# Kernel optimization log

Measured on AMD Instinct MI355X. Metric: run time of the kernel, lower is better.

Reference implementation:

```python
import jax, jax.numpy as jnp
import numpy as np

DIM = -1
ALPHA = 1.5
N_ITERS = 100


def _p(z):
    # p(z) = clamp(z, min=0) ** (1 / (alpha - 1)); for alpha=1.5 this is square
    return jnp.maximum(z, 0.0) ** (1.0 / (ALPHA - 1.0))


def entmax_bisect(X):
    """Bisection search for the entmax threshold tau (entmax_bisect, alpha=1.5)."""
    am1 = ALPHA - 1.0
    d = X.shape[DIM]
    Xs = X * am1                                   # scaled logits
    max_val = jnp.max(Xs, axis=DIM, keepdims=True)
    tau_lo = max_val - 1.0                         # gp(1) = 1**(alpha-1) = 1
    tau_hi = max_val - (1.0 / d) ** am1            # gp(1/d)
    f_lo = jnp.sum(_p(Xs - tau_lo), axis=DIM, keepdims=True) - 1.0
    dm0 = tau_hi - tau_lo

    def body(i, carry):
        tau_lo, dm, _ = carry
        dm = dm * 0.5
        tau_m = tau_lo + dm
        p_m = _p(Xs - tau_m)
        f_m = jnp.sum(p_m, axis=DIM, keepdims=True) - 1.0
        tau_lo = jnp.where(f_m * f_lo >= 0.0, tau_m, tau_lo)
        return (tau_lo, dm, p_m)

    p0 = jnp.zeros_like(Xs)
    _, _, p_m = jax.lax.fori_loop(0, N_ITERS, body, (tau_lo, dm0, p0))
    # ensure_sum_one normalization (as in the entmax library forward)
    return p_m / jnp.sum(p_m, axis=DIM, keepdims=True)


def setup_inputs() -> dict:
    key = jax.random.key(0)
    x = jax.random.normal(key, (2, 1024, 32000), dtype=jnp.float32)
    return {"x": x}


def reference(x):
    # LogEntmaxBisect.forward: log(entmax_bisect(x, dim, alpha, iters))
    # zero-probability entries yield -inf, matching torch.log(0.)
    return jnp.log(entmax_bisect(x))
```

## Files before the change

### kernel.cpp

```cpp
#include <hip/hip_runtime.h>
#include <float.h>
#include <math.h>

#define D_DIM   32000
#define NT      256
#define CHUNKS  (D_DIM / 4)
#define KITER   ((CHUNKS + NT - 1) / NT)
#define NG4     (KITER / 4)
#define NWAVES  (NT / 64)
#define CAPW    1200

typedef float f32x4 __attribute__((ext_vector_type(4)));
typedef unsigned long long ull;

__device__ __forceinline__ float waveReduceSum(float v) {
#pragma unroll
    for (int m = 32; m >= 1; m >>= 1) v += __shfl_xor(v, m, 64);
    return v;
}

__device__ __forceinline__ float waveReduceMax(float v) {
#pragma unroll
    for (int m = 32; m >= 1; m >>= 1) v = fmaxf(v, __shfl_xor(v, m, 64));
    return v;
}

__device__ __forceinline__ float scrub_finite(float v) {
    const unsigned u = __float_as_uint(v);
    if ((u & 0x7f800000u) == 0x7f800000u) return -FLT_MAX;
    return v;
}

__device__ __forceinline__ float4 ldg4(const float4* __restrict__ p, int c) {
    if (c < CHUNKS) return p[c];
    float4 r; r.x = r.y = r.z = r.w = -FLT_MAX;
    return r;
}

__global__ __launch_bounds__(NT, 8)
void entmax_log_fused(const float* __restrict__ x, float* __restrict__ out, int rows)
{
    const int row = blockIdx.x;
    if (row >= rows) return;
    const size_t base = (size_t)row * D_DIM;
    const float4* __restrict__ xr4 = reinterpret_cast<const float4*>(x + base);
    float* __restrict__ orow = out + base;

    __shared__ __align__(16) float s_pool[NWAVES * CAPW];
    __shared__ float s_red[NWAVES];
    __shared__ int   s_cnt[NWAVES];
    __shared__ int   s_flag;
    __shared__ float2 s_ts;

    const int lane = threadIdx.x & 63;
    const int wv   = threadIdx.x >> 6;
    float* __restrict__ wpool = s_pool + wv * CAPW;
    const ull lmask = (1ull << lane) - 1ull;

    if (threadIdx.x == 0) s_flag = 0;
    __syncthreads();

    float runL  = -FLT_MAX;
    float waveM = -FLT_MAX;
    float pendR = -FLT_MAX;
    int n = 0;
    bool ovf = false;

    float4 cur[4], nxt[4];
#pragma unroll
    for (int j = 0; j < 4; ++j) cur[j] = ldg4(xr4, threadIdx.x + j * NT);

    for (int g = 0; g < NG4; ++g) {
        if (g + 1 < NG4) {
#pragma unroll
            for (int j = 0; j < 4; ++j)
                nxt[j] = ldg4(xr4, threadIdx.x + ((g + 1) * 4 + j) * NT);
        }
        float z[16];
#pragma unroll
        for (int j = 0; j < 4; ++j) {
            z[4 * j + 0] = cur[j].x; z[4 * j + 1] = cur[j].y;
            z[4 * j + 2] = cur[j].z; z[4 * j + 3] = cur[j].w;
        }
        float cm = z[0];
#pragma unroll
        for (int i = 1; i < 16; ++i) cm = fmaxf(cm, z[i]);
        runL = fmaxf(runL, cm);
        if ((g & 1) == 0) {
            waveM = fmaxf(waveM, pendR);
            pendR = waveReduceMax(runL);
        }

        float thrL = fmaxf(runL, waveM) - 2.0f;
        ull msk[16];
        int tot = 0;
#pragma unroll
        for (int j = 0; j < 16; ++j) {
            msk[j] = __ballot(z[j] > thrL);
            tot += __popcll(msk[j]);
        }
        if (tot) {
            if (n + tot > CAPW) {
                const float wfresh = waveReduceMax(runL);
                waveM = fmaxf(waveM, wfresh);
                const float thrW = wfresh - 2.0f;
                int nn = 0;
                for (int i = 0; i < n; i += 64) {
                    const float v = (i + lane < n) ? wpool[i + lane] : -FLT_MAX;
                    const ull km = __ballot(v > thrW);
                    const int r = __popcll(km & lmask);
                    if (v > thrW) wpool[nn + r] = v;
                    nn += __popcll(km);
                }
                n = nn;
                thrL = fmaxf(runL, waveM) - 2.0f;
                tot = 0;
#pragma unroll
                for (int j = 0; j < 16; ++j) {
                    msk[j] = __ballot(z[j] > thrL);
                    tot += __popcll(msk[j]);
                }
            }
            if (n + tot > CAPW) {
                ovf = true;
            } else {
#pragma unroll
                for (int j = 0; j < 16; ++j) {
                    if (z[j] > thrL) {
                        const int r = __popcll(msk[j] & lmask);
                        wpool[n + r] = z[j];
                    }
                    n += __popcll(msk[j]);
                }
            }
        }
#pragma unroll
        for (int j = 0; j < 4; ++j) cur[j] = nxt[j];
    }
    if (ovf && lane == 0) s_flag = 1;

    if (lane == 0) s_red[wv] = waveReduceMax(runL);
    __syncthreads();
    const float max_val = fmaxf(fmaxf(s_red[0], s_red[1]), fmaxf(s_red[2], s_red[3]));
    const int flag = s_flag;
    __syncthreads();

    const float u_lo0 = max_val - 2.0f;
    const float u_hi  = max_val - 0.011180339887498949f;

    if (!flag) {
        {
            int nn = 0;
            for (int i = 0; i < n; i += 64) {
                const float v = (i + lane < n) ? wpool[i + lane] : -FLT_MAX;
                const ull km = __ballot(v > u_lo0);
                const int r = __popcll(km & lmask);
                if (v > u_lo0) wpool[nn + r] = v;
                nn += __popcll(km);
            }
            if (lane == 0) s_cnt[wv] = nn;
        }
        __syncthreads();

        if (wv == 0) {
            const int n0 = s_cnt[0], n1 = s_cnt[1], n2 = s_cnt[2], n3 = s_cnt[3];

#define POOL_SCAN(uv, acc)                                                     \
            do {                                                               \
                const float* __restrict__ pp0 = s_pool;                        \
                for (int i = lane; i < n0; i += 64) {                          \
                    const float t = fmaxf(pp0[i] - (uv), 0.0f);                \
                    acc = fmaf(t, t, acc);                                     \
                }                                                              \
                const float* __restrict__ pp1 = s_pool + CAPW;                 \
                for (int i = lane; i < n1; i += 64) {                          \
                    const float t = fmaxf(pp1[i] - (uv), 0.0f);                \
                    acc = fmaf(t, t, acc);                                     \
                }                                                              \
                const float* __restrict__ pp2 = s_pool + 2 * CAPW;             \
                for (int i = lane; i < n2; i += 64) {                          \
                    const float t = fmaxf(pp2[i] - (uv), 0.0f);                \
                    acc = fmaf(t, t, acc);                                     \
                }                                                              \
                const float* __restrict__ pp3 = s_pool + 3 * CAPW;             \
                for (int i = lane; i < n3; i += 64) {                          \
                    const float t = fmaxf(pp3[i] - (uv), 0.0f);                \
                    acc = fmaf(t, t, acc);                                     \
                }                                                              \
            } while (0)

            float u_lo = u_lo0;
            float fl = 0.0f;
            POOL_SCAN(u_lo, fl);
            fl = waveReduceSum(fl) - 4.0f;

            float dm = u_hi - u_lo;
            float u_m = u_lo;
            float s_v = 4.0f;
            for (int it = 0; it < 100; ++it) {
                dm *= 0.5f;
                u_m = u_lo + dm;
                const bool fixed = (u_m == u_lo);
                float a = 0.0f;
                POOL_SCAN(u_m, a);
                a = waveReduceSum(a);
                s_v = a;
                if ((a - 4.0f) * fl >= 0.0f) u_lo = u_m;
                if (fixed) break;
            }
#undef POOL_SCAN
            if (lane == 0) { s_ts.x = u_m; s_ts.y = s_v; }
        }
        __syncthreads();
    } else {
        float u_lo = u_lo0;
        float acc = 0.0f;
        for (int k = 0; k < KITER; ++k) {
            const int c = threadIdx.x + k * NT;
            if (c < CHUNKS) {
                const float4 v = xr4[c];
                float t;
                t = fmaxf(v.x - u_lo, 0.0f); acc = fmaf(t, t, acc);
                t = fmaxf(v.y - u_lo, 0.0f); acc = fmaf(t, t, acc);
                t = fmaxf(v.z - u_lo, 0.0f); acc = fmaf(t, t, acc);
                t = fmaxf(v.w - u_lo, 0.0f); acc = fmaf(t, t, acc);
            }
        }
        acc = waveReduceSum(acc);
        if (lane == 0) s_red[wv] = acc;
        __syncthreads();
        const float f_lo = (s_red[0] + s_red[1] + s_red[2] + s_red[3]) - 4.0f;
        __syncthreads();

        float dm = u_hi - u_lo;
        float u_m = u_lo;
        float s_v = 4.0f;
        for (int it = 0; it < 100; ++it) {
            dm *= 0.5f;
            u_m = u_lo + dm;
            const bool fixed = (u_m == u_lo);
            float a = 0.0f;
            for (int k = 0; k < KITER; ++k) {
                const int c = threadIdx.x + k * NT;
                if (c < CHUNKS) {
                    const float4 v = xr4[c];
                    float t;
                    t = fmaxf(v.x - u_m, 0.0f); a = fmaf(t, t, a);
                    t = fmaxf(v.y - u_m, 0.0f); a = fmaf(t, t, a);
                    t = fmaxf(v.z - u_m, 0.0f); a = fmaf(t, t, a);
                    t = fmaxf(v.w - u_m, 0.0f); a = fmaf(t, t, a);
                }
            }
            a = waveReduceSum(a);
            if (lane == 0) s_red[wv] = a;
            __syncthreads();
            const float s = s_red[0] + s_red[1] + s_red[2] + s_red[3];
            __syncthreads();
            s_v = s;
            if ((s - 4.0f) * f_lo >= 0.0f) u_lo = u_m;
            if (fixed) break;
        }
        if (threadIdx.x == 0) { s_ts.x = u_m; s_ts.y = s_v; }
        __syncthreads();
    }

    const float u_m = s_ts.x;
    const float inv_sv = 1.0f / s_ts.y;
    for (int k = 0; k < KITER; ++k) {
        const int c = threadIdx.x + k * NT;
        if (c < CHUNKS) {
            const float4 v = xr4[c];
            f32x4 o;
            {
                const float t = fmaxf(v.x - u_m, 0.0f);
                o.x = scrub_finite(__logf(fmaxf(t * t, 1e-35f) * inv_sv));
            }
            {
                const float t = fmaxf(v.y - u_m, 0.0f);
                o.y = scrub_finite(__logf(fmaxf(t * t, 1e-35f) * inv_sv));
            }
            {
                const float t = fmaxf(v.z - u_m, 0.0f);
                o.z = scrub_finite(__logf(fmaxf(t * t, 1e-35f) * inv_sv));
            }
            {
                const float t = fmaxf(v.w - u_m, 0.0f);
                o.w = scrub_finite(__logf(fmaxf(t * t, 1e-35f) * inv_sv));
            }
            __builtin_nontemporal_store(o, reinterpret_cast<f32x4*>(orow) + c);
        }
    }
}

extern "C" void kernel_launch(void* const* d_in, const int* in_sizes, int n_in,
                              void* d_out, int out_size, void* d_ws, size_t ws_size,
                              hipStream_t stream) {
    const float* x = (const float*)d_in[0];
    float* out = (float*)d_out;
    const int rows = in_sizes[0] / D_DIM;
    entmax_log_fused<<<dim3(rows), dim3(NT), 0, stream>>>(x, out, rows);
}
```

Measured before the change: 145.3 us.

## Replace pool bisection with Newton iteration on threshold; nontemporal loads in output pass

On the pooled-candidate path, the up-to-100-step bisection is replaced by a Newton iteration that accumulates both sum(t^2) and sum(t) per pass and steps the threshold by g/(2*S1), clamped at u_hi, for at most 24 iterations. This aims to cut the number of serial single-wave scans over the shared pool. The final normalisation and log pass now reads the input with nontemporal loads. The result is no longer the bisection midpoint the reference produces, so it depends on Newton converging monotonically from below on this piecewise-quadratic function.

```diff
diff --git a/kernel.cpp b/kernel.cpp
--- a/kernel.cpp
+++ b/kernel.cpp
@@ -165,51 +165,46 @@
         if (wv == 0) {
             const int n0 = s_cnt[0], n1 = s_cnt[1], n2 = s_cnt[2], n3 = s_cnt[3];
 
-#define POOL_SCAN(uv, acc)                                                     \
+#define POOL_SCAN2(uv, acc2, acc1)                                             \
             do {                                                               \
                 const float* __restrict__ pp0 = s_pool;                        \
                 for (int i = lane; i < n0; i += 64) {                          \
                     const float t = fmaxf(pp0[i] - (uv), 0.0f);                \
-                    acc = fmaf(t, t, acc);                                     \
+                    acc2 = fmaf(t, t, acc2); acc1 += t;                        \
                 }                                                              \
                 const float* __restrict__ pp1 = s_pool + CAPW;                 \
                 for (int i = lane; i < n1; i += 64) {                          \
                     const float t = fmaxf(pp1[i] - (uv), 0.0f);                \
-                    acc = fmaf(t, t, acc);                                     \
+                    acc2 = fmaf(t, t, acc2); acc1 += t;                        \
                 }                                                              \
                 const float* __restrict__ pp2 = s_pool + 2 * CAPW;             \
                 for (int i = lane; i < n2; i += 64) {                          \
                     const float t = fmaxf(pp2[i] - (uv), 0.0f);                \
-                    acc = fmaf(t, t, acc);                                     \
+                    acc2 = fmaf(t, t, acc2); acc1 += t;                        \
                 }                                                              \
                 const float* __restrict__ pp3 = s_pool + 3 * CAPW;             \
                 for (int i = lane; i < n3; i += 64) {                          \
                     const float t = fmaxf(pp3[i] - (uv), 0.0f);                \
-                    acc = fmaf(t, t, acc);                                     \
+                    acc2 = fmaf(t, t, acc2); acc1 += t;                        \
                 }                                                              \
             } while (0)
 
-            float u_lo = u_lo0;
-            float fl = 0.0f;
-            POOL_SCAN(u_lo, fl);
-            fl = waveReduceSum(fl) - 4.0f;
-
-            float dm = u_hi - u_lo;
-            float u_m = u_lo;
+            float u = u_lo0;
             float s_v = 4.0f;
-            for (int it = 0; it < 100; ++it) {
-                dm *= 0.5f;
-                u_m = u_lo + dm;
-                const bool fixed = (u_m == u_lo);
-                float a = 0.0f;
-                POOL_SCAN(u_m, a);
-                a = waveReduceSum(a);
-                s_v = a;
-                if ((a - 4.0f) * fl >= 0.0f) u_lo = u_m;
-                if (fixed) break;
-            }
-#undef POOL_SCAN
-            if (lane == 0) { s_ts.x = u_m; s_ts.y = s_v; }
+            for (int it = 0; it < 24; ++it) {
+                float S2 = 0.0f, S1 = 0.0f;
+                POOL_SCAN2(u, S2, S1);
+                S2 = waveReduceSum(S2);
+                S1 = waveReduceSum(S1);
+                s_v = S2;
+                const float g = S2 - 4.0f;
+                if (g <= 0.0f) break;
+                const float u_new = fminf(u + g / (2.0f * S1), u_hi);
+                if (u_new == u) break;
+                u = u_new;
+            }
+#undef POOL_SCAN2
+            if (lane == 0) { s_ts.x = u; s_ts.y = s_v; }
         }
         __syncthreads();
     } else {
@@ -266,10 +261,11 @@
 
     const float u_m = s_ts.x;
     const float inv_sv = 1.0f / s_ts.y;
+    const f32x4* __restrict__ xv4 = reinterpret_cast<const f32x4*>(x + base);
     for (int k = 0; k < KITER; ++k) {
         const int c = threadIdx.x + k * NT;
         if (c < CHUNKS) {
-            const float4 v = xr4[c];
+            const f32x4 v = __builtin_nontemporal_load(xv4 + c);
             f32x4 o;
             {
                 const float t = fmaxf(v.x - u_m, 0.0f);
```

After: 127.6 us. 1.14x faster.
